# Kernel tuning notes

Hardware: AMD Instinct MI355X
Metric: run time of the kernel (lower is better)

Reference implementation:

```python
import jax, jax.numpy as jnp
import numpy as np

NUM_Q = 1000
DIM_S = 64
SIZE_M = 50
BATCH = 128
SEQ = 200


def setup_inputs() -> dict:
    key = jax.random.key(0)
    ks = jax.random.split(key, 16)
    s = 1.0 / np.sqrt(DIM_S)
    inp = {
        "q": jax.random.randint(ks[0], (BATCH, SEQ), 0, NUM_Q),
        "r": jax.random.randint(ks[1], (BATCH, SEQ), 0, 2),
        "at_s": jax.random.randint(ks[2], (BATCH, 16), 0, 30000),
        "at_m": jnp.ones((BATCH, 16), dtype=jnp.int64 if jax.config.jax_enable_x64 else jnp.int32),
        "k_emb": jax.random.normal(ks[3], (NUM_Q, DIM_S)) * s,
        "v_emb": jax.random.normal(ks[4], (2 * NUM_Q, DIM_S)) * s,
        "Mk": jax.random.normal(ks[5], (SIZE_M, DIM_S)) * s,
        "Mv0": jax.random.normal(ks[6], (SIZE_M, DIM_S)) * s,
        "We": jax.random.normal(ks[7], (DIM_S, DIM_S)) * s,
        "be": jnp.zeros((DIM_S,)),
        "Wa": jax.random.normal(ks[8], (DIM_S, DIM_S)) * s,
        "ba": jnp.zeros((DIM_S,)),
        "Wf": jax.random.normal(ks[9], (2 * DIM_S, DIM_S)) * s,
        "bf": jnp.zeros((DIM_S,)),
        "Wp": jax.random.normal(ks[10], (DIM_S, 1)) * s,
        "bp": jnp.zeros((1,)),
    }
    return inp


def reference(q, r, at_s, at_m, k_emb, v_emb, Mk, Mv0, We, be, Wa, ba, Wf, bf, Wp, bp):
    num_q = k_emb.shape[0]
    x = q + r * num_q                         # [B, n]
    k = k_emb[q]                              # [B, n, d]
    v = v_emb[x]                              # [B, n, d]
    w = jax.nn.softmax(jnp.einsum("bnd,md->bnm", k, Mk), axis=-1)  # [B, n, m]
    e = jax.nn.sigmoid(v @ We + be)           # erase gate [B, n, d]
    a = jnp.tanh(v @ Wa + ba)                 # add vector [B, n, d]

    B = q.shape[0]
    Mv_init = jnp.broadcast_to(Mv0[None], (B,) + Mv0.shape)  # [B, m, d]

    def step(Mvt, inp):
        et, at_, wt = inp                     # [B,d], [B,d], [B,m]
        Mvt = Mvt * (1.0 - wt[:, :, None] * et[:, None, :]) + wt[:, :, None] * at_[:, None, :]
        return Mvt, Mvt

    xs = (e.transpose(1, 0, 2), a.transpose(1, 0, 2), w.transpose(1, 0, 2))
    _, Mv_seq = jax.lax.scan(step, Mv_init, xs)             # [n, B, m, d]
    Mv = jnp.concatenate([Mv_init[None], Mv_seq], axis=0)   # [n+1, B, m, d]
    Mv = Mv.transpose(1, 0, 2, 3)                            # [B, n+1, m, d]

    read = jnp.einsum("bnm,bnmd->bnd", w, Mv[:, :-1])        # read from pre-update memory
    f = jnp.tanh(jnp.concatenate([read, k], axis=-1) @ Wf + bf)
    p = jax.nn.sigmoid((f @ Wp + bp)).squeeze(-1)            # [B, n]; dropout is identity at eval
    return p, Mv
```

## Files before the change

kernel.cpp:

```cpp
#include <hip/hip_runtime.h>
#include <hip/hip_bf16.h>

typedef __hip_bfloat16 bf16;

#define BATCH 128
#define SEQ   200
#define NUMQ  1000
#define DD    64
#define MM    50
#define CHUNKS 10
#define CLEN   20


__device__ __forceinline__ float rdlane(float v, int j) {
    return __uint_as_float(__builtin_amdgcn_readlane(__float_as_uint(v), j));
}

__global__ __launch_bounds__(256) void k1_precompute(
    const int* __restrict__ q, const int* __restrict__ r,
    const float* __restrict__ k_emb, const float* __restrict__ v_emb,
    const float* __restrict__ Mk,
    const float* __restrict__ We, const float* __restrict__ be,
    const float* __restrict__ Wa, const float* __restrict__ ba,
    float* __restrict__ w_buf, float* __restrict__ e_buf, float* __restrict__ a_buf)
{
    __shared__ float Mk_l[MM][DD + 1];
    __shared__ float kv_l[4][128];

    const int tid = threadIdx.x;
    for (int i = tid; i < MM * DD; i += 256)
        Mk_l[i >> 6][i & 63] = Mk[i];

    const int w    = tid >> 6;
    const int lane = tid & 63;
    const int row  = blockIdx.x * 4 + w;

    int qi = q[row], ri = r[row];
    qi = min(max(qi, 0), NUMQ - 1);
    ri = min(max(ri, 0), 1);
    const int xi = qi + ri * NUMQ;

    kv_l[w][lane]      = k_emb[(size_t)qi * DD + lane];
    kv_l[w][64 + lane] = v_emb[(size_t)xi * DD + lane];
    __syncthreads();

    float s = 0.f;
    if (lane < MM) {
        #pragma unroll
        for (int dd = 0; dd < DD; ++dd)
            s += kv_l[w][dd] * Mk_l[lane][dd];
    }
    float mx = (lane < MM) ? s : -1e30f;
    #pragma unroll
    for (int off = 32; off >= 1; off >>= 1)
        mx = fmaxf(mx, __shfl_xor(mx, off, 64));
    float ex = (lane < MM) ? expf(s - mx) : 0.f;
    float sm = ex;
    #pragma unroll
    for (int off = 32; off >= 1; off >>= 1)
        sm += __shfl_xor(sm, off, 64);
    if (lane < MM)
        w_buf[(size_t)row * MM + lane] = ex / sm;

    float ea = be[lane], aa = ba[lane];
    #pragma unroll
    for (int dd = 0; dd < DD; ++dd) {
        const float vb = kv_l[w][64 + dd];
        ea = __builtin_fmaf(vb, We[dd * DD + lane], ea);
        aa = __builtin_fmaf(vb, Wa[dd * DD + lane], aa);
    }
    e_buf[(size_t)row * DD + lane] = 1.f / (1.f + expf(-ea));
    a_buf[(size_t)row * DD + lane] = tanhf(aa);
}

__global__ __launch_bounds__(64) void k2_scan_chunked(
    const float* __restrict__ Mv0,
    const float* __restrict__ w_buf, const float* __restrict__ e_buf,
    const float* __restrict__ a_buf,
    float* __restrict__ read_buf, float* __restrict__ out_Mv)
{
    const int bid  = blockIdx.x;
    const int b    = bid / CHUNKS;
    const int c    = bid % CHUNKS;
    const int lane = threadIdx.x;
    const int t0   = c * CLEN;

    float Mv[MM];
    float* outb = out_Mv + (size_t)b * (SEQ + 1) * MM * DD;
    #pragma unroll
    for (int j = 0; j < MM; ++j)
        Mv[j] = Mv0[j * DD + lane];
    if (c == 0) {
        #pragma unroll
        for (int j = 0; j < MM; ++j)
            outb[j * DD + lane] = Mv[j];
    }

    const float* wrow = w_buf + (size_t)b * SEQ * MM;
    const float* erow = e_buf + (size_t)b * SEQ * DD;
    const float* arow = a_buf + (size_t)b * SEQ * DD;
    float*       rrow = read_buf + (size_t)b * SEQ * DD;

    float wreg = (lane < MM) ? wrow[lane] : 0.f;
    float e_n  = erow[lane];
    float a_n  = arow[lane];

    for (int t = 0; t < t0; ++t) {
        const float e_v = e_n, a_v = a_n, wcur = wreg;
        wreg = (lane < MM) ? wrow[(size_t)(t + 1) * MM + lane] : 0.f;
        e_n  = erow[(size_t)(t + 1) * DD + lane];
        a_n  = arow[(size_t)(t + 1) * DD + lane];
        #pragma unroll
        for (int j = 0; j < MM; ++j) {
            const float wj = rdlane(wcur, j);
            Mv[j] = __builtin_fmaf(wj, __builtin_fmaf(-e_v, Mv[j], a_v), Mv[j]);
        }
    }

    for (int tt = 0; tt < CLEN; ++tt) {
        const int t = t0 + tt;
        const float e_v = e_n, a_v = a_n, wcur = wreg;
        if (t + 1 < SEQ) {
            wreg = (lane < MM) ? wrow[(size_t)(t + 1) * MM + lane] : 0.f;
            e_n  = erow[(size_t)(t + 1) * DD + lane];
            a_n  = arow[(size_t)(t + 1) * DD + lane];
        }
        float* outt = outb + (size_t)(t + 1) * MM * DD;
        float racc0 = 0.f, racc1 = 0.f;
        #pragma unroll
        for (int j = 0; j < MM; ++j) {
            const float wj    = rdlane(wcur, j);
            const float m_old = Mv[j];
            if (j & 1) racc1 = __builtin_fmaf(wj, m_old, racc1);
            else       racc0 = __builtin_fmaf(wj, m_old, racc0);
            Mv[j] = __builtin_fmaf(wj, __builtin_fmaf(-e_v, m_old, a_v), m_old);
            outt[j * DD + lane] = Mv[j];
        }
        rrow[(size_t)t * DD + lane] = racc0 + racc1;
    }
}

__global__ __launch_bounds__(256) void k3_out(
    const int* __restrict__ q,
    const float* __restrict__ k_emb,
    const float* __restrict__ read_buf,
    const float* __restrict__ Wf, const float* __restrict__ bfb,
    const float* __restrict__ Wp, const float* __restrict__ bp,
    float* __restrict__ out_p)
{
    __shared__ float rk[4][128];
    const int tid  = threadIdx.x;
    const int w    = tid >> 6;
    const int lane = tid & 63;
    const int row  = blockIdx.x * 4 + w;

    int qi = q[row];
    qi = min(max(qi, 0), NUMQ - 1);
    rk[w][lane]      = read_buf[(size_t)row * DD + lane];
    rk[w][64 + lane] = k_emb[(size_t)qi * DD + lane];
    __syncthreads();

    float acc = bfb[lane];
    #pragma unroll
    for (int i = 0; i < 2 * DD; ++i)
        acc = __builtin_fmaf(rk[w][i], Wf[i * DD + lane], acc);
    const float f = tanhf(acc);

    float pv = f * Wp[lane];
    #pragma unroll
    for (int off = 32; off >= 1; off >>= 1)
        pv += __shfl_xor(pv, off, 64);

    if (lane == 0)
        out_p[row] = 1.f / (1.f + expf(-(pv + bp[0])));
}

__global__ __launch_bounds__(640) void dkvmn_fused(
    const int* q_, const int* r_,
    const float* k_emb, const float* v_emb, const float* Mk, const float* Mv0,
    const float* We, const float* be, const float* Wa, const float* ba,
    const float* Wf, const float* bfb, const float* Wp, const float* bp,
    float* out_p, float* out_Mv)
{
    __shared__ float Mk_l[MM][DD + 1];
    __shared__ bf16  ring[SEQ][DD];
    __shared__ int   q_row[SEQ], x_row[SEQ];
    __shared__ float kbuf[DD], vbuf[DD], vbuf2[DD];
    __shared__ float wst[MM], est[DD], ast[DD];
    __shared__ float partial[640];
    __shared__ float bias_e[DD], bias_a[DD];

    const int b    = blockIdx.x;
    const int tid  = threadIdx.x;
    const int wv   = tid >> 6;
    const int lane = tid & 63;

    for (int t = tid; t < SEQ; t += 640) {
        int qi = q_[b * SEQ + t], ri = r_[b * SEQ + t];
        qi = min(max(qi, 0), NUMQ - 1); ri = min(max(ri, 0), 1);
        q_row[t] = qi; x_row[t] = qi + ri * NUMQ;
    }
    for (int i = tid; i < MM * DD; i += 640) Mk_l[i >> 6][i & 63] = Mk[i];
    if (tid < DD) { bias_e[tid] = be[tid]; bias_a[tid] = ba[tid]; }

    const int d  = lane;
    const int m0 = wv * 5;
    float* outb = out_Mv + (size_t)b * (SEQ + 1) * MM * DD;
    float Mv[5];
    #pragma unroll
    for (int j = 0; j < 5; ++j) {
        Mv[j] = Mv0[(m0 + j) * DD + d];
        outb[(m0 + j) * DD + d] = Mv[j];
    }
    __syncthreads();

    float kf_n = 0.f, vf_n = 0.f, vf2_n = 0.f;
    if (wv == 0) kf_n  = k_emb[(size_t)q_row[0] * DD + lane];
    if (wv == 1) vf_n  = v_emb[(size_t)x_row[0] * DD + lane];
    if (wv == 2) vf2_n = v_emb[(size_t)x_row[0] * DD + lane];

    for (int t = 0; t < SEQ; ++t) {
        if (wv == 0) {
            kbuf[lane] = kf_n;
            if (t + 1 < SEQ) kf_n = k_emb[(size_t)q_row[t + 1] * DD + lane];
            float s = 0.f;
            if (lane < MM) {
                #pragma unroll
                for (int dd = 0; dd < DD; ++dd) s += kbuf[dd] * Mk_l[lane][dd];
            }
            float mx = (lane < MM) ? s : -1e30f;
            #pragma unroll
            for (int off = 32; off >= 1; off >>= 1) mx = fmaxf(mx, __shfl_xor(mx, off, 64));
            float ex = (lane < MM) ? expf(s - mx) : 0.f;
            float sm = ex;
            #pragma unroll
            for (int off = 32; off >= 1; off >>= 1) sm += __shfl_xor(sm, off, 64);
            if (lane < MM) wst[lane] = ex / sm;
        } else if (wv == 1) {
            vbuf[lane] = vf_n;
            if (t + 1 < SEQ) vf_n = v_emb[(size_t)x_row[t + 1] * DD + lane];
            float acc = bias_e[lane];
            #pragma unroll
            for (int dd = 0; dd < DD; ++dd) acc += vbuf[dd] * We[dd * DD + lane];
            est[lane] = 1.f / (1.f + expf(-acc));
        } else if (wv == 2) {
            vbuf2[lane] = vf2_n;
            if (t + 1 < SEQ) vf2_n = v_emb[(size_t)x_row[t + 1] * DD + lane];
            float acc = bias_a[lane];
            #pragma unroll
            for (int dd = 0; dd < DD; ++dd) acc += vbuf2[dd] * Wa[dd * DD + lane];
            ast[lane] = tanhf(acc);
        }
        __syncthreads();

        const float e_v = est[d];
        const float a_v = ast[d];
        float racc = 0.f;
        float* outt = outb + (size_t)(t + 1) * MM * DD;
        #pragma unroll
        for (int j = 0; j < 5; ++j) {
            const float wvv = wst[m0 + j];
            racc += wvv * Mv[j];
            Mv[j] = __builtin_fmaf(wvv, a_v - e_v * Mv[j], Mv[j]);
            outt[(m0 + j) * DD + d] = Mv[j];
        }
        partial[tid] = racc;
        __syncthreads();

        if (tid < DD) {
            float rr = 0.f;
            #pragma unroll
            for (int g = 0; g < 10; ++g) rr += partial[g * 64 + tid];
            ring[t][tid] = (bf16)rr;
        }
    }
    __syncthreads();

    for (int t = wv; t < SEQ; t += 10) {
        const int qi = q_row[t];
        const float kreg = k_emb[(size_t)qi * DD + lane];
        float acc = bfb[lane];
        #pragma unroll
        for (int i = 0; i < DD; ++i) acc += (float)ring[t][i] * Wf[i * DD + lane];
        #pragma unroll
        for (int i = 0; i < DD; ++i) acc += __shfl(kreg, i, 64) * Wf[(DD + i) * DD + lane];
        const float f = tanhf(acc);
        float pv = f * Wp[lane];
        #pragma unroll
        for (int off = 32; off >= 1; off >>= 1) pv += __shfl_xor(pv, off, 64);
        if (lane == 0)
            out_p[(size_t)b * SEQ + t] = 1.f / (1.f + expf(-(pv + bp[0])));
    }
}

extern "C" void kernel_launch(void* const* d_in, const int* in_sizes, int n_in,
                              void* d_out, int out_size, void* d_ws, size_t ws_size,
                              hipStream_t stream) {
    const int*   q     = (const int*)  d_in[0];
    const int*   r     = (const int*)  d_in[1];
    const float* k_emb = (const float*)d_in[4];
    const float* v_emb = (const float*)d_in[5];
    const float* Mk    = (const float*)d_in[6];
    const float* Mv0   = (const float*)d_in[7];
    const float* We    = (const float*)d_in[8];
    const float* be    = (const float*)d_in[9];
    const float* Wa    = (const float*)d_in[10];
    const float* ba    = (const float*)d_in[11];
    const float* Wf    = (const float*)d_in[12];
    const float* bfb   = (const float*)d_in[13];
    const float* Wp    = (const float*)d_in[14];
    const float* bp    = (const float*)d_in[15];

    float* out_p  = (float*)d_out;
    float* out_Mv = (float*)d_out + BATCH * SEQ;

    const size_t WS_NEEDED = (size_t)BATCH * SEQ * (MM + 3 * DD) * sizeof(float);

    if (ws_size >= WS_NEEDED) {
        float* w_buf    = (float*)d_ws;
        float* e_buf    = w_buf + (size_t)BATCH * SEQ * MM;
        float* a_buf    = e_buf + (size_t)BATCH * SEQ * DD;
        float* read_buf = a_buf + (size_t)BATCH * SEQ * DD;

        const int rows = BATCH * SEQ;

        hipLaunchKernelGGL(k1_precompute, dim3(rows / 4), dim3(256), 0, stream,
                           q, r, k_emb, v_emb, Mk, We, be, Wa, ba, w_buf, e_buf, a_buf);
        hipLaunchKernelGGL(k2_scan_chunked, dim3(BATCH * CHUNKS), dim3(64), 0, stream,
                           Mv0, w_buf, e_buf, a_buf, read_buf, out_Mv);
        hipLaunchKernelGGL(k3_out, dim3(rows / 4), dim3(256), 0, stream,
                           q, k_emb, read_buf, Wf, bfb, Wp, bp, out_p);
    } else {
        hipLaunchKernelGGL(dkvmn_fused, dim3(BATCH), dim3(640), 0, stream,
                           q, r, k_emb, v_emb, Mk, Mv0, We, be, Wa, ba,
                           Wf, bfb, Wp, bp, out_p, out_Mv);
    }
}
```

Measured before the change: 189.8 us.

## Replace chunked scan with two-pass summary and replay affine scan

Splits the memory recurrence into two kernels. The first computes, for each chunk, the combined affine transform (product of erase factors and the accumulated add term). The second composes the summaries of all prior chunks to get each chunk's starting memory, then replays its own chunk while writing Mv and read vectors. This aims to remove the serial dependency or inter-block waiting of the prior chunked scan, at the cost of an extra kernel launch, extra workspace traffic and a second pass over w/e/a. It applies only when the workspace is large enough.

After: 184.0 us. 3.1% less time.

```diff
diff --git a/kernel.cpp b/kernel.cpp
--- a/kernel.cpp
+++ b/kernel.cpp
@@ -71,6 +71,120 @@
     }
     e_buf[(size_t)row * DD + lane] = 1.f / (1.f + expf(-ea));
     a_buf[(size_t)row * DD + lane] = tanhf(aa);
+}
+
+__global__ __launch_bounds__(64) void k2a_summary(
+    const float* __restrict__ w_buf, const float* __restrict__ e_buf,
+    const float* __restrict__ a_buf,
+    float* __restrict__ Abuf, float* __restrict__ Bbuf)
+{
+    const int bid  = blockIdx.x;
+    const int b    = bid / CHUNKS;
+    const int c    = bid % CHUNKS;
+    const int lane = threadIdx.x;
+    const int t0   = c * CLEN;
+
+    const float* wrow = w_buf + (size_t)b * SEQ * MM;
+    const float* erow = e_buf + (size_t)b * SEQ * DD;
+    const float* arow = a_buf + (size_t)b * SEQ * DD;
+
+    float A[MM], B[MM];
+    #pragma unroll
+    for (int j = 0; j < MM; ++j) { A[j] = 1.f; B[j] = 0.f; }
+
+    float wreg = (lane < MM) ? wrow[(size_t)t0 * MM + lane] : 0.f;
+    float e_n  = erow[(size_t)t0 * DD + lane];
+    float a_n  = arow[(size_t)t0 * DD + lane];
+
+    for (int tt = 0; tt < CLEN; ++tt) {
+        const int t = t0 + tt;
+        const float e_v = e_n, a_v = a_n, wcur = wreg;
+        if (t + 1 < SEQ) {
+            wreg = (lane < MM) ? wrow[(size_t)(t + 1) * MM + lane] : 0.f;
+            e_n  = erow[(size_t)(t + 1) * DD + lane];
+            a_n  = arow[(size_t)(t + 1) * DD + lane];
+        }
+        #pragma unroll
+        for (int j = 0; j < MM; ++j) {
+            const float wj = rdlane(wcur, j);
+            const float f  = __builtin_fmaf(-wj, e_v, 1.f);
+            const float g  = wj * a_v;
+            A[j] *= f;
+            B[j] = __builtin_fmaf(B[j], f, g);
+        }
+    }
+
+    float* Ao = Abuf + ((size_t)bid * MM) * DD;
+    float* Bo = Bbuf + ((size_t)bid * MM) * DD;
+    #pragma unroll
+    for (int j = 0; j < MM; ++j) {
+        Ao[j * DD + lane] = A[j];
+        Bo[j * DD + lane] = B[j];
+    }
+}
+
+__global__ __launch_bounds__(64) void k2c_replay(
+    const float* __restrict__ Mv0,
+    const float* __restrict__ w_buf, const float* __restrict__ e_buf,
+    const float* __restrict__ a_buf,
+    const float* __restrict__ Abuf, const float* __restrict__ Bbuf,
+    float* __restrict__ read_buf, float* __restrict__ out_Mv)
+{
+    const int bid  = blockIdx.x;
+    const int b    = bid / CHUNKS;
+    const int c    = bid % CHUNKS;
+    const int lane = threadIdx.x;
+    const int t0   = c * CLEN;
+
+    float Mv[MM];
+    float* outb = out_Mv + (size_t)b * (SEQ + 1) * MM * DD;
+    #pragma unroll
+    for (int j = 0; j < MM; ++j)
+        Mv[j] = Mv0[j * DD + lane];
+    if (c == 0) {
+        #pragma unroll
+        for (int j = 0; j < MM; ++j)
+            outb[j * DD + lane] = Mv[j];
+    }
+
+    for (int cc = 0; cc < c; ++cc) {
+        const float* Ao = Abuf + ((size_t)(b * CHUNKS + cc) * MM) * DD;
+        const float* Bo = Bbuf + ((size_t)(b * CHUNKS + cc) * MM) * DD;
+        #pragma unroll
+        for (int j = 0; j < MM; ++j)
+            Mv[j] = __builtin_fmaf(Ao[j * DD + lane], Mv[j], Bo[j * DD + lane]);
+    }
+
+    const float* wrow = w_buf + (size_t)b * SEQ * MM;
+    const float* erow = e_buf + (size_t)b * SEQ * DD;
+    const float* arow = a_buf + (size_t)b * SEQ * DD;
+    float*       rrow = read_buf + (size_t)b * SEQ * DD;
+
+    float wreg = (lane < MM) ? wrow[(size_t)t0 * MM + lane] : 0.f;
+    float e_n  = erow[(size_t)t0 * DD + lane];
+    float a_n  = arow[(size_t)t0 * DD + lane];
+
+    for (int tt = 0; tt < CLEN; ++tt) {
+        const int t = t0 + tt;
+        const float e_v = e_n, a_v = a_n, wcur = wreg;
+        if (t + 1 < SEQ) {
+            wreg = (lane < MM) ? wrow[(size_t)(t + 1) * MM + lane] : 0.f;
+            e_n  = erow[(size_t)(t + 1) * DD + lane];
+            a_n  = arow[(size_t)(t + 1) * DD + lane];
+        }
+        float* outt = outb + (size_t)(t + 1) * MM * DD;
+        float racc0 = 0.f, racc1 = 0.f;
+        #pragma unroll
+        for (int j = 0; j < MM; ++j) {
+            const float wj    = rdlane(wcur, j);
+            const float m_old = Mv[j];
+            if (j & 1) racc1 = __builtin_fmaf(wj, m_old, racc1);
+            else       racc0 = __builtin_fmaf(wj, m_old, racc0);
+            Mv[j] = __builtin_fmaf(wj, __builtin_fmaf(-e_v, m_old, a_v), m_old);
+            outt[j * DD + lane] = Mv[j];
+        }
+        rrow[(size_t)t * DD + lane] = racc0 + racc1;
+    }
 }
 
 __global__ __launch_bounds__(64) void k2_scan_chunked(
@@ -314,20 +428,34 @@
     float* out_p  = (float*)d_out;
     float* out_Mv = (float*)d_out + BATCH * SEQ;
 
-    const size_t WS_NEEDED = (size_t)BATCH * SEQ * (MM + 3 * DD) * sizeof(float);
-
-    if (ws_size >= WS_NEEDED) {
+    const size_t N_WEA  = (size_t)BATCH * SEQ * (MM + 3 * DD);
+    const size_t N_SUM  = (size_t)BATCH * CHUNKS * MM * DD;
+    const size_t WS_BASE = N_WEA * sizeof(float);
+    const size_t WS_HIER = WS_BASE + 2 * N_SUM * sizeof(float);
+
+    const int rows = BATCH * SEQ;
+
+    if (ws_size >= WS_BASE) {
         float* w_buf    = (float*)d_ws;
         float* e_buf    = w_buf + (size_t)BATCH * SEQ * MM;
         float* a_buf    = e_buf + (size_t)BATCH * SEQ * DD;
         float* read_buf = a_buf + (size_t)BATCH * SEQ * DD;
 
-        const int rows = BATCH * SEQ;
-
         hipLaunchKernelGGL(k1_precompute, dim3(rows / 4), dim3(256), 0, stream,
                            q, r, k_emb, v_emb, Mk, We, be, Wa, ba, w_buf, e_buf, a_buf);
-        hipLaunchKernelGGL(k2_scan_chunked, dim3(BATCH * CHUNKS), dim3(64), 0, stream,
-                           Mv0, w_buf, e_buf, a_buf, read_buf, out_Mv);
+
+        if (ws_size >= WS_HIER) {
+            float* Abuf = read_buf + (size_t)BATCH * SEQ * DD;
+            float* Bbuf = Abuf + N_SUM;
+            hipLaunchKernelGGL(k2a_summary, dim3(BATCH * CHUNKS), dim3(64), 0, stream,
+                               w_buf, e_buf, a_buf, Abuf, Bbuf);
+            hipLaunchKernelGGL(k2c_replay, dim3(BATCH * CHUNKS), dim3(64), 0, stream,
+                               Mv0, w_buf, e_buf, a_buf, Abuf, Bbuf, read_buf, out_Mv);
+        } else {
+            hipLaunchKernelGGL(k2_scan_chunked, dim3(BATCH * CHUNKS), dim3(64), 0, stream,
+                               Mv0, w_buf, e_buf, a_buf, read_buf, out_Mv);
+        }
+
         hipLaunchKernelGGL(k3_out, dim3(rows / 4), dim3(256), 0, stream,
                            q, k_emb, read_buf, Wf, bfb, Wp, bp, out_p);
     } else {
```

## Replace redundant chunk prefix replay with hierarchical affine scan over memory halves

Applied to the files above, without the earlier changes.

Each chunk previously replayed every earlier timestep to rebuild its starting memory, so later chunks did quadratic redundant work. Now each wave folds its chunk into a per-slot affine map (A,B), the chunk start states are passed sequentially through shared memory, and each wave then replays only its own chunk. Memory slots are also split into two halves across blocks, so the read output becomes two partial sums that k3 adds together. Stores of the memory history are made nontemporal. The cost is an extra pass over the chunk, ten serialized syncthreads steps, and a larger workspace.

New measurement: 155.8 us. 1.22x faster.

```diff
diff --git a/kernel.cpp b/kernel.cpp
--- a/kernel.cpp
+++ b/kernel.cpp
@@ -8,6 +8,7 @@
 #define NUMQ  1000
 #define DD    64
 #define MM    50
+#define MH    25
 #define CHUNKS 10
 #define CLEN   20
 
@@ -73,68 +74,99 @@
     a_buf[(size_t)row * DD + lane] = tanhf(aa);
 }
 
-__global__ __launch_bounds__(64) void k2_scan_chunked(
+__global__ __launch_bounds__(640) void k2_hier(
     const float* __restrict__ Mv0,
     const float* __restrict__ w_buf, const float* __restrict__ e_buf,
     const float* __restrict__ a_buf,
-    float* __restrict__ read_buf, float* __restrict__ out_Mv)
+    float* __restrict__ read2_buf, float* __restrict__ out_Mv)
 {
-    const int bid  = blockIdx.x;
-    const int b    = bid / CHUNKS;
-    const int c    = bid % CHUNKS;
-    const int lane = threadIdx.x;
-    const int t0   = c * CLEN;
-
-    float Mv[MM];
-    float* outb = out_Mv + (size_t)b * (SEQ + 1) * MM * DD;
-    #pragma unroll
-    for (int j = 0; j < MM; ++j)
-        Mv[j] = Mv0[j * DD + lane];
-    if (c == 0) {
-        #pragma unroll
-        for (int j = 0; j < MM; ++j)
-            outb[j * DD + lane] = Mv[j];
-    }
-
-    const float* wrow = w_buf + (size_t)b * SEQ * MM;
+    __shared__ float S[MH][DD];
+
+    const int blk  = blockIdx.x;
+    const int b    = blk >> 1;
+    const int h    = blk & 1;
+    const int tid  = threadIdx.x;
+    const int wv   = tid >> 6;
+    const int lane = tid & 63;
+    const int t0   = wv * CLEN;
+    const int mb   = h * MH;
+
+    const float* wrow = w_buf + (size_t)b * SEQ * MM + mb;
     const float* erow = e_buf + (size_t)b * SEQ * DD;
     const float* arow = a_buf + (size_t)b * SEQ * DD;
-    float*       rrow = read_buf + (size_t)b * SEQ * DD;
-
-    float wreg = (lane < MM) ? wrow[lane] : 0.f;
-    float e_n  = erow[lane];
-    float a_n  = arow[lane];
-
-    for (int t = 0; t < t0; ++t) {
-        const float e_v = e_n, a_v = a_n, wcur = wreg;
-        wreg = (lane < MM) ? wrow[(size_t)(t + 1) * MM + lane] : 0.f;
-        e_n  = erow[(size_t)(t + 1) * DD + lane];
-        a_n  = arow[(size_t)(t + 1) * DD + lane];
-        #pragma unroll
-        for (int j = 0; j < MM; ++j) {
-            const float wj = rdlane(wcur, j);
-            Mv[j] = __builtin_fmaf(wj, __builtin_fmaf(-e_v, Mv[j], a_v), Mv[j]);
-        }
-    }
+
+    float A[MH], B[MH];
+    #pragma unroll
+    for (int j = 0; j < MH; ++j) { A[j] = 1.f; B[j] = 0.f; }
+
+    float wreg = (lane < MH) ? wrow[(size_t)t0 * MM + lane] : 0.f;
+    float e_n  = erow[(size_t)t0 * DD + lane];
+    float a_n  = arow[(size_t)t0 * DD + lane];
 
     for (int tt = 0; tt < CLEN; ++tt) {
         const int t = t0 + tt;
         const float e_v = e_n, a_v = a_n, wcur = wreg;
         if (t + 1 < SEQ) {
-            wreg = (lane < MM) ? wrow[(size_t)(t + 1) * MM + lane] : 0.f;
+            wreg = (lane < MH) ? wrow[(size_t)(t + 1) * MM + lane] : 0.f;
             e_n  = erow[(size_t)(t + 1) * DD + lane];
             a_n  = arow[(size_t)(t + 1) * DD + lane];
         }
+        #pragma unroll
+        for (int j = 0; j < MH; ++j) {
+            const float wj = rdlane(wcur, j);
+            const float f  = __builtin_fmaf(-wj, e_v, 1.f);
+            A[j] *= f;
+            B[j] = __builtin_fmaf(B[j], f, wj * a_v);
+        }
+    }
+
+    float* outb = out_Mv + (size_t)b * (SEQ + 1) * MM * DD + (size_t)mb * DD;
+    if (wv == 0) {
+        #pragma unroll
+        for (int j = 0; j < MH; ++j) {
+            const float m0v = Mv0[(mb + j) * DD + lane];
+            S[j][lane] = m0v;
+            __builtin_nontemporal_store(m0v, &outb[j * DD + lane]);
+        }
+    }
+    __syncthreads();
+
+    float Mv[MH];
+    for (int w = 0; w < CHUNKS; ++w) {
+        if (wv == w) {
+            #pragma unroll
+            for (int j = 0; j < MH; ++j) {
+                Mv[j] = S[j][lane];
+                S[j][lane] = __builtin_fmaf(A[j], Mv[j], B[j]);
+            }
+        }
+        __syncthreads();
+    }
+
+    float* rrow = read2_buf + ((size_t)h * BATCH + b) * SEQ * DD;
+
+    wreg = (lane < MH) ? wrow[(size_t)t0 * MM + lane] : 0.f;
+    e_n  = erow[(size_t)t0 * DD + lane];
+    a_n  = arow[(size_t)t0 * DD + lane];
+
+    for (int tt = 0; tt < CLEN; ++tt) {
+        const int t = t0 + tt;
+        const float e_v = e_n, a_v = a_n, wcur = wreg;
+        if (t + 1 < SEQ) {
+            wreg = (lane < MH) ? wrow[(size_t)(t + 1) * MM + lane] : 0.f;
+            e_n  = erow[(size_t)(t + 1) * DD + lane];
+            a_n  = arow[(size_t)(t + 1) * DD + lane];
+        }
         float* outt = outb + (size_t)(t + 1) * MM * DD;
         float racc0 = 0.f, racc1 = 0.f;
         #pragma unroll
-        for (int j = 0; j < MM; ++j) {
+        for (int j = 0; j < MH; ++j) {
             const float wj    = rdlane(wcur, j);
             const float m_old = Mv[j];
             if (j & 1) racc1 = __builtin_fmaf(wj, m_old, racc1);
             else       racc0 = __builtin_fmaf(wj, m_old, racc0);
             Mv[j] = __builtin_fmaf(wj, __builtin_fmaf(-e_v, m_old, a_v), m_old);
-            outt[j * DD + lane] = Mv[j];
+            __builtin_nontemporal_store(Mv[j], &outt[j * DD + lane]);
         }
         rrow[(size_t)t * DD + lane] = racc0 + racc1;
     }
@@ -143,7 +175,7 @@
 __global__ __launch_bounds__(256) void k3_out(
     const int* __restrict__ q,
     const float* __restrict__ k_emb,
-    const float* __restrict__ read_buf,
+    const float* __restrict__ read2_buf,
     const float* __restrict__ Wf, const float* __restrict__ bfb,
     const float* __restrict__ Wp, const float* __restrict__ bp,
     float* __restrict__ out_p)
@@ -156,7 +188,10 @@
 
     int qi = q[row];
     qi = min(max(qi, 0), NUMQ - 1);
-    rk[w][lane]      = read_buf[(size_t)row * DD + lane];
+
+    const float* rd0 = read2_buf;
+    const float* rd1 = read2_buf + (size_t)BATCH * SEQ * DD;
+    rk[w][lane]      = rd0[(size_t)row * DD + lane] + rd1[(size_t)row * DD + lane];
     rk[w][64 + lane] = k_emb[(size_t)qi * DD + lane];
     __syncthreads();
 
@@ -314,22 +349,24 @@
     float* out_p  = (float*)d_out;
     float* out_Mv = (float*)d_out + BATCH * SEQ;
 
-    const size_t WS_NEEDED = (size_t)BATCH * SEQ * (MM + 3 * DD) * sizeof(float);
+    const size_t N_W  = (size_t)BATCH * SEQ * MM;
+    const size_t N_D  = (size_t)BATCH * SEQ * DD;
+    const size_t WS_NEEDED = (N_W + 4 * N_D) * sizeof(float);
+
+    const int rows = BATCH * SEQ;
 
     if (ws_size >= WS_NEEDED) {
-        float* w_buf    = (float*)d_ws;
-        float* e_buf    = w_buf + (size_t)BATCH * SEQ * MM;
-        float* a_buf    = e_buf + (size_t)BATCH * SEQ * DD;
-        float* read_buf = a_buf + (size_t)BATCH * SEQ * DD;
-
-        const int rows = BATCH * SEQ;
+        float* w_buf     = (float*)d_ws;
+        float* e_buf     = w_buf + N_W;
+        float* a_buf     = e_buf + N_D;
+        float* read2_buf = a_buf + N_D;
 
         hipLaunchKernelGGL(k1_precompute, dim3(rows / 4), dim3(256), 0, stream,
                            q, r, k_emb, v_emb, Mk, We, be, Wa, ba, w_buf, e_buf, a_buf);
-        hipLaunchKernelGGL(k2_scan_chunked, dim3(BATCH * CHUNKS), dim3(64), 0, stream,
-                           Mv0, w_buf, e_buf, a_buf, read_buf, out_Mv);
+        hipLaunchKernelGGL(k2_hier, dim3(BATCH * 2), dim3(640), 0, stream,
+                           Mv0, w_buf, e_buf, a_buf, read2_buf, out_Mv);
         hipLaunchKernelGGL(k3_out, dim3(rows / 4), dim3(256), 0, stream,
-                           q, k_emb, read_buf, Wf, bfb, Wp, bp, out_p);
+                           q, k_emb, read2_buf, Wf, bfb, Wp, bp, out_p);
     } else {
         hipLaunchKernelGGL(dkvmn_fused, dim3(BATCH), dim3(640), 0, stream,
                            q, r, k_emb, v_emb, Mk, Mv0, We, be, Wa, ba,
```
